# Optimization experiments

Measured on AMD Instinct MI355X. Metric: run time of the kernel, lower is better.

## Reference

```python
import jax, jax.numpy as jnp
import numpy as np

B, N, S, C, H = 16, 64, 4096, 768, 1
HEAD_DIM = C // H
SCALE = HEAD_DIM ** -0.5
ASSIGN_EPS = 1.0


def setup_inputs() -> dict:
    key = jax.random.key(0)
    ks = jax.random.split(key, 8)
    w = lambda k: jax.random.normal(k, (C, C), jnp.float32) * 0.02
    return {
        "query": jax.random.normal(ks[0], (B, N, C), jnp.float32),       # group tokens
        "key_tokens": jax.random.normal(ks[1], (B, S, C), jnp.float32),  # sequence tokens
        "Wq": w(ks[2]), "bq": jnp.zeros((C,), jnp.float32),
        "Wk": w(ks[3]), "bk": jnp.zeros((C,), jnp.float32),
        "Wv": w(ks[4]), "bv": jnp.zeros((C,), jnp.float32),
        "Wo": w(ks[5]), "bo": jnp.zeros((C,), jnp.float32),
    }


def reference(query, key_tokens, Wq, bq, Wk, bk, Wv, bv, Wo, bo):
    # AssignAttention forward (hard=True, gumbel=False -> hard_softmax path).
    def split_heads(x):  # [b, t, C] -> [b, h, t, c]
        b, t, _ = x.shape
        return x.reshape(b, t, H, HEAD_DIM).transpose(0, 2, 1, 3)

    q = split_heads(query @ Wq.T + bq)        # [B, H, N, c]
    k = split_heads(key_tokens @ Wk.T + bk)   # [B, H, S, c]
    v = split_heads(key_tokens @ Wv.T + bv)   # [B, H, S, c]

    raw_attn = jnp.einsum('bhnc,bhsc->bhns', q, k) * SCALE  # [B, H, N, S]

    # hard_softmax over the group (query) dim, axis=-2, with straight-through estimator
    y_soft = jax.nn.softmax(raw_attn, axis=-2)
    idx = jnp.argmax(y_soft, axis=-2)                          # [B, H, S]
    y_hard = jnp.swapaxes(jax.nn.one_hot(idx, N, dtype=raw_attn.dtype), -1, -2)  # [B, H, N, S]
    attn = jax.lax.stop_gradient(y_hard - y_soft) + y_soft

    # sum-renormalization over assigned tokens (sum_assign=False)
    attn = attn / (attn.sum(axis=-1, keepdims=True) + ASSIGN_EPS)

    out = jnp.einsum('bhns,bhsc->bhnc', attn, v)  # [B, H, N, c]
    out = out.transpose(0, 2, 1, 3).reshape(B, N, C)
    return out @ Wo.T + bo
```

## Files before the change

### kernel.cpp

```cpp
#include <hip/hip_runtime.h>
#include <hip/hip_bf16.h>

#define BQ 16
#define NG 64
#define SQ 4096
#define CD 768
#define ROWS (BQ*NG)
#define KSP 4

__global__ __launch_bounds__(256)
void transpose64(const float* __restrict__ src, float* __restrict__ dst,
                 int M, int N)
{
    __shared__ float t[64][65];
    const int bx = blockIdx.x * 64;
    const int by = blockIdx.y * 64;
    const int tx = threadIdx.x & 63, tw = threadIdx.x >> 6;
#pragma unroll
    for (int i = 0; i < 16; ++i) {
        const int row = i * 4 + tw;
        t[row][tx] = src[(size_t)(by + row) * N + bx + tx];
    }
    __syncthreads();
#pragma unroll
    for (int i = 0; i < 16; ++i) {
        const int row = i * 4 + tw;
        dst[(size_t)(bx + row) * M + by + tx] = t[tx][row];
    }
}

__global__ __launch_bounds__(256)
void vecmat3(const float* __restrict__ Wq, const float* __restrict__ bk,
             const float* __restrict__ Wk, const float* __restrict__ bq,
             const float* __restrict__ WoT, const float* __restrict__ bv,
             float* __restrict__ uq, float* __restrict__ bqk,
             float* __restrict__ bvo)
{
    __shared__ float red[4][64];
    const float* Mm; const float* v; float* out;
    if (blockIdx.y == 0)      { Mm = Wq;  v = bk; out = uq;  }
    else if (blockIdx.y == 1) { Mm = Wk;  v = bq; out = bqk; }
    else                      { Mm = WoT; v = bv; out = bvo; }
    const int j0 = blockIdx.x * 64;
    const int jl = threadIdx.x & 63;
    const int cs = threadIdx.x >> 6;
    double a = 0.0;
    for (int c = cs; c < CD; c += 4)
        a += (double)Mm[(size_t)c * CD + j0 + jl] * (double)v[c];
    red[cs][jl] = (float)a;
    __syncthreads();
    if (cs == 0) out[j0 + jl] = red[0][jl] + red[1][jl] + red[2][jl] + red[3][jl];
}

__global__ __launch_bounds__(256)
void delta_q(const float* __restrict__ query, const float* __restrict__ uq,
             const float* __restrict__ bq, const float* __restrict__ bk,
             double* __restrict__ delta)
{
    const int r    = blockIdx.x * 4 + (threadIdx.x >> 6);
    const int lane = threadIdx.x & 63;
    double a = 0.0, b = 0.0;
    for (int c = lane; c < CD; c += 64) {
        a += (double)query[(size_t)r * CD + c] * (double)uq[c];
        b += (double)bq[c] * (double)bk[c];
    }
    a += b;
    for (int off = 32; off; off >>= 1) a += __shfl_down(a, off, 64);
    if (lane == 0) delta[r] = a;
}

__device__ __forceinline__
void gemm_core(const float* __restrict__ AT, int lda,
               const float* __restrict__ B,  int ldb,
               float* __restrict__ Pz, int r0, int c0, int k0, int prow0)
{
    __shared__ float As[64][72];
    __shared__ float Bs[64][72];
    const int tid = threadIdx.x;
    const int c4  = tid & 15;
    const int kr  = tid >> 4;
    const int cg  = tid & 15;
    const int rg  = tid >> 4;

    float  acc[4][4]; double acc64[4][4];
#pragma unroll
    for (int i = 0; i < 4; ++i)
#pragma unroll
        for (int j = 0; j < 4; ++j) { acc[i][j] = 0.f; acc64[i][j] = 0.0; }

    for (int ch = 0; ch < 3; ++ch) {
        const int kb = k0 + ch * 64;
        if (ch) __syncthreads();
#pragma unroll
        for (int i = 0; i < 4; ++i) {
            const int row = i * 16 + kr;
            *(float4*)&As[row][4 * c4] = *(const float4*)(AT + (size_t)(kb + row) * lda + r0 + 4 * c4);
            *(float4*)&Bs[row][4 * c4] = *(const float4*)(B  + (size_t)(kb + row) * ldb + c0 + 4 * c4);
        }
        __syncthreads();
#pragma unroll 8
        for (int dd = 0; dd < 64; ++dd) {
            const float4 a = *(const float4*)&As[dd][4 * rg];
            const float4 b = *(const float4*)&Bs[dd][4 * cg];
            const float av[4] = {a.x, a.y, a.z, a.w};
            const float bv[4] = {b.x, b.y, b.z, b.w};
#pragma unroll
            for (int i = 0; i < 4; ++i)
#pragma unroll
                for (int j = 0; j < 4; ++j) acc[i][j] += av[i] * bv[j];
        }
#pragma unroll
        for (int i = 0; i < 4; ++i)
#pragma unroll
            for (int j = 0; j < 4; ++j) { acc64[i][j] += (double)acc[i][j]; acc[i][j] = 0.f; }
    }
#pragma unroll
    for (int i = 0; i < 4; ++i) {
        const int row = prow0 + 4 * rg + i;
        float4 v;
        v.x = (float)acc64[i][0]; v.y = (float)acc64[i][1];
        v.z = (float)acc64[i][2]; v.w = (float)acc64[i][3];
        *(float4*)(Pz + (size_t)row * CD + c0 + 4 * cg) = v;
    }
}

__global__ __launch_bounds__(256)
void gemm_w(const float* __restrict__ Wq, const float* __restrict__ Wk,
            const float* __restrict__ Wv, const float* __restrict__ WoT,
            float* __restrict__ P)
{
    const int by = blockIdx.y;
    float* Pz = P + (size_t)blockIdx.z * (1536 * CD);
    const float* AT; const float* Bp; int r0;
    if (by < 12) { AT = Wq; Bp = Wk;  r0 = by * 64; }
    else         { AT = Wv; Bp = WoT; r0 = (by - 12) * 64; }
    gemm_core(AT, CD, Bp, CD, Pz, r0, blockIdx.x * 64, blockIdx.z * 192, by * 64);
}

__global__ __launch_bounds__(256)
void gemm_d(const float* __restrict__ AT, const float* __restrict__ B,
            float* __restrict__ P)
{
    float* Pz = P + (size_t)blockIdx.z * (ROWS * CD);
    const int r0 = blockIdx.y * 64;
    gemm_core(AT, ROWS, B, CD, Pz, r0, blockIdx.x * 64, blockIdx.z * 192, r0);
}

__global__ __launch_bounds__(256)
void reduce_sk(const float* __restrict__ P, const float* __restrict__ bias,
               const float* __restrict__ bias2, const int* __restrict__ cnt,
               float* __restrict__ out, int M, int mode)
{
    const int e = blockIdx.x * 256 + threadIdx.x;
    if (e >= M * CD) return;
    const size_t MN = (size_t)M * CD;
    double a = 0.0;
#pragma unroll
    for (int z = 0; z < KSP; ++z) a += (double)P[z * MN + e];
    float v = (float)a;
    if (mode == 1) v += bias[e % CD];
    else if (mode == 3) {
        const int r = e / CD;
        const int cv = cnt[r];
        const float invf = 1.f / ((float)cv + 1.f);
        v = v * invf + ((float)cv * invf) * bias2[e % CD] + bias[e % CD];
    }
    out[e] = v;
}

struct ScoreTiles { float As[64][64]; float Bs[128][64]; };
struct ScoreRed   { double bval[128][17]; int bidx[128][17]; };
union  ScoreShared { ScoreTiles t; ScoreRed r; };

__global__ __launch_bounds__(256)
void score_argmax(const float* __restrict__ gT, const float* __restrict__ key,
                  const double* __restrict__ delta, int* __restrict__ idxo)
{
    __shared__ ScoreShared sh;
    const int tid = threadIdx.x;
    const int b   = blockIdx.y;
    const int s0  = blockIdx.x * 128;
    const int sg  = tid & 15;
    const int ng  = tid >> 4;
    const int c4  = tid & 15;
    const int t4  = tid >> 4;

    float  acc[4][8]; double acc64[4][8];
#pragma unroll
    for (int i = 0; i < 4; ++i)
#pragma unroll
        for (int j = 0; j < 8; ++j) { acc[i][j] = 0.f; acc64[i][j] = 0.0; }

    const float* keyb = key + ((size_t)b * SQ + s0) * CD;
    const float* gTb  = gT + (size_t)b * 64;

    for (int t = 0; t < 12; ++t) {
        const int kb = t * 64;
        __syncthreads();
#pragma unroll
        for (int it = 0; it < 8; ++it) {
            const int row = it * 16 + t4;
            const float4 v = *(const float4*)(keyb + (size_t)row * CD + kb + 4 * c4);
            *(float4*)&sh.t.Bs[row][4 * ((c4 ^ (row >> 3)) & 15)] = v;
        }
#pragma unroll
        for (int it = 0; it < 4; ++it) {
            const int row = it * 16 + t4;
            const float4 v = *(const float4*)(gTb + (size_t)(kb + row) * ROWS + 4 * c4);
            *(float4*)&sh.t.As[row][4 * c4] = v;
        }
        __syncthreads();
#pragma unroll 2
        for (int ddq = 0; ddq < 16; ++ddq) {
            float4 kf[8];
#pragma unroll
            for (int j = 0; j < 8; ++j)
                kf[j] = *(const float4*)&sh.t.Bs[8 * sg + j][4 * ((ddq ^ sg) & 15)];
#pragma unroll
            for (int d = 0; d < 4; ++d) {
                const float4 a = *(const float4*)&sh.t.As[4 * ddq + d][4 * ng];
                const float av[4] = { a.x, a.y, a.z, a.w };
#pragma unroll
                for (int j = 0; j < 8; ++j) {
                    const float kd = (d == 0) ? kf[j].x : (d == 1) ? kf[j].y
                                   : (d == 2) ? kf[j].z : kf[j].w;
#pragma unroll
                    for (int i = 0; i < 4; ++i) acc[i][j] += av[i] * kd;
                }
            }
        }
#pragma unroll
        for (int i = 0; i < 4; ++i)
#pragma unroll
            for (int j = 0; j < 8; ++j) { acc64[i][j] += (double)acc[i][j]; acc[i][j] = 0.f; }
    }

    double dl[4];
#pragma unroll
    for (int i = 0; i < 4; ++i) dl[i] = delta[b * 64 + 4 * ng + i];

    double bv[8]; int bn[8];
#pragma unroll
    for (int j = 0; j < 8; ++j) {
        bv[j] = acc64[0][j] + dl[0]; bn[j] = 4 * ng;
#pragma unroll
        for (int i = 1; i < 4; ++i) {
            const double v = acc64[i][j] + dl[i];
            if (v > bv[j]) { bv[j] = v; bn[j] = 4 * ng + i; }
        }
    }
    __syncthreads();
#pragma unroll
    for (int j = 0; j < 8; ++j) {
        sh.r.bval[8 * sg + j][ng] = bv[j];
        sh.r.bidx[8 * sg + j][ng] = bn[j];
    }
    __syncthreads();
    if (tid < 128) {
        const int s = tid;
        double best = sh.r.bval[s][0]; int bi = sh.r.bidx[s][0];
#pragma unroll
        for (int k = 1; k < 16; ++k) {
            const double v = sh.r.bval[s][k];
            if (v > best) { best = v; bi = sh.r.bidx[s][k]; }
        }
        idxo[b * SQ + s0 + s] = bi;
    }
}

__global__ __launch_bounds__(256)
void gather_ksum(const float* __restrict__ key, const int* __restrict__ idx,
                 float* __restrict__ Ksum, int* __restrict__ cnt)
{
    __shared__ int slist[SQ];
    __shared__ int scount;
    const int n   = blockIdx.x;
    const int b   = blockIdx.y;
    const int tid = threadIdx.x;
    if (tid == 0) scount = 0;
    __syncthreads();

    const int* ib = idx + b * SQ;
#pragma unroll
    for (int p = 0; p < SQ / 256; ++p) {
        const int s = p * 256 + tid;
        if (ib[s] == n) {
            const int pos = atomicAdd(&scount, 1);
            slist[pos] = s;
        }
    }
    __syncthreads();
    const int m = scount;

    double a0 = 0.0, a1 = 0.0, a2 = 0.0;
    const float* kb = key + (size_t)b * SQ * CD;
    const int c1 = tid + 256, c2 = tid + 512;

    int r = 0;
    for (; r + 4 <= m; r += 4) {
        const float* p0 = kb + (size_t)slist[r]     * CD;
        const float* p1 = kb + (size_t)slist[r + 1] * CD;
        const float* p2 = kb + (size_t)slist[r + 2] * CD;
        const float* p3 = kb + (size_t)slist[r + 3] * CD;
        a0 += (double)p0[tid] + (double)p1[tid] + (double)p2[tid] + (double)p3[tid];
        a1 += (double)p0[c1] + (double)p1[c1] + (double)p2[c1] + (double)p3[c1];
        a2 += (double)p0[c2] + (double)p1[c2] + (double)p2[c2] + (double)p3[c2];
    }
    for (; r < m; ++r) {
        const float* p0 = kb + (size_t)slist[r] * CD;
        a0 += (double)p0[tid]; a1 += (double)p0[c1]; a2 += (double)p0[c2];
    }

    float* out = Ksum + (size_t)(b * 64 + n) * CD;
    out[tid] = (float)a0; out[c1] = (float)a1; out[c2] = (float)a2;
    if (tid == 0) cnt[b * 64 + n] = m;
}

extern "C" void kernel_launch(void* const* d_in, const int* in_sizes, int n_in,
                              void* d_out, int out_size, void* d_ws, size_t ws_size,
                              hipStream_t stream)
{
    const float* query = (const float*)d_in[0];
    const float* key   = (const float*)d_in[1];
    const float* Wq    = (const float*)d_in[2];
    const float* bq    = (const float*)d_in[3];
    const float* Wk    = (const float*)d_in[4];
    const float* bk    = (const float*)d_in[5];
    const float* Wv    = (const float*)d_in[6];
    const float* bv    = (const float*)d_in[7];
    const float* Wo    = (const float*)d_in[8];
    const float* bo    = (const float*)d_in[9];

    char* ws = (char*)d_ws;
    const size_t MB = 1 << 20;
    int*    cnt   = (int*)   (ws + 0);
    double* delta = (double*)(ws + 4096);
    float*  uq    = (float*) (ws + 16384);
    float*  bqk   = (float*) (ws + 19456);
    float*  bvo   = (float*) (ws + 22528);
    int*    idx   = (int*)   (ws + 32768);
    float*  qT    = (float*) (ws + 1 * MB);
    float*  WoT   = (float*) (ws + 4 * MB);
    float*  Wqk   = (float*) (ws + 7 * MB);
    float*  Wvo   = Wqk + 768 * 768;
    float*  g     = (float*) (ws + 12 * MB);
    float*  Ksum  = (float*) (ws + 15 * MB);
    float*  KsumT = (float*) (ws + 18 * MB);
    float*  P     = (float*) (ws + 21 * MB);

    transpose64<<<dim3(12, 12), 256, 0, stream>>>(Wo, WoT, CD, CD);
    transpose64<<<dim3(12, 16), 256, 0, stream>>>(query, qT, ROWS, CD);
    vecmat3<<<dim3(12, 3), 256, 0, stream>>>(Wq, bk, Wk, bq, WoT, bv, uq, bqk, bvo);
    delta_q<<<ROWS / 4, 256, 0, stream>>>(query, uq, bq, bk, delta);
    gemm_w<<<dim3(12, 24, KSP), 256, 0, stream>>>(Wq, Wk, Wv, WoT, P);
    reduce_sk<<<(1536 * CD) / 256, 256, 0, stream>>>(P, nullptr, nullptr, nullptr, Wqk, 1536, 0);
    gemm_d<<<dim3(12, 16, KSP), 256, 0, stream>>>(qT, Wqk, P);
    reduce_sk<<<(ROWS * CD) / 256, 256, 0, stream>>>(P, bqk, nullptr, nullptr, g, ROWS, 1);
    float* gT = qT;
    transpose64<<<dim3(12, 16), 256, 0, stream>>>(g, gT, ROWS, CD);
    score_argmax<<<dim3(SQ / 128, BQ), 256, 0, stream>>>(gT, key, delta, idx);
    gather_ksum<<<dim3(NG, BQ), 256, 0, stream>>>(key, idx, Ksum, cnt);
    transpose64<<<dim3(12, 16), 256, 0, stream>>>(Ksum, KsumT, ROWS, CD);
    gemm_d<<<dim3(12, 16, KSP), 256, 0, stream>>>(KsumT, Wvo, P);
    reduce_sk<<<(ROWS * CD) / 256, 256, 0, stream>>>(P, bo, bvo, cnt, (float*)d_out, ROWS, 3);
}
```

Baseline: 643.2 us.

## Rewrite score_argmax with register-resident query slices and per-wave channel split

```diff
diff --git a/kernel.cpp b/kernel.cpp
--- a/kernel.cpp
+++ b/kernel.cpp
@@ -168,103 +168,65 @@
     out[e] = v;
 }
 
-struct ScoreTiles { float As[64][64]; float Bs[128][64]; };
-struct ScoreRed   { double bval[128][17]; int bidx[128][17]; };
-union  ScoreShared { ScoreTiles t; ScoreRed r; };
-
-__global__ __launch_bounds__(256)
+#define STILE 256
+#define SB    16
+
+__global__ __launch_bounds__(768)
 void score_argmax(const float* __restrict__ gT, const float* __restrict__ key,
                   const double* __restrict__ delta, int* __restrict__ idxo)
 {
-    __shared__ ScoreShared sh;
+    __shared__ float  part[SB][12][64];
+    __shared__ double sc[SB][65];
+    __shared__ double dl[64];
+
     const int tid = threadIdx.x;
     const int b   = blockIdx.y;
-    const int s0  = blockIdx.x * 128;
-    const int sg  = tid & 15;
-    const int ng  = tid >> 4;
-    const int c4  = tid & 15;
-    const int t4  = tid >> 4;
-
-    float  acc[4][8]; double acc64[4][8];
-#pragma unroll
-    for (int i = 0; i < 4; ++i)
-#pragma unroll
-        for (int j = 0; j < 8; ++j) { acc[i][j] = 0.f; acc64[i][j] = 0.0; }
-
-    const float* keyb = key + ((size_t)b * SQ + s0) * CD;
-    const float* gTb  = gT + (size_t)b * 64;
-
-    for (int t = 0; t < 12; ++t) {
-        const int kb = t * 64;
+    const int s0  = blockIdx.x * STILE;
+    const int w   = __builtin_amdgcn_readfirstlane(tid >> 6);
+    const int l   = tid & 63;
+
+    if (tid < 64) dl[tid] = delta[b * 64 + tid];
+
+    float greg[64];
+#pragma unroll
+    for (int kk = 0; kk < 64; ++kk)
+        greg[kk] = gT[(size_t)(w * 64 + kk) * ROWS + b * 64 + l];
+
+    const float* keyb = key + (size_t)b * SQ * CD + (size_t)w * 64;
+
+    __syncthreads();
+
+    for (int sb = 0; sb < STILE; sb += SB) {
+        for (int si = 0; si < SB; ++si) {
+            const float* kp = keyb + (size_t)(s0 + sb + si) * CD;
+            float a = 0.f;
+#pragma unroll
+            for (int q = 0; q < 16; ++q) {
+                const float4 kv = *(const float4*)(kp + 4 * q);
+                a += greg[4 * q + 0] * kv.x;
+                a += greg[4 * q + 1] * kv.y;
+                a += greg[4 * q + 2] * kv.z;
+                a += greg[4 * q + 3] * kv.w;
+            }
+            part[si][w][l] = a;
+        }
         __syncthreads();
-#pragma unroll
-        for (int it = 0; it < 8; ++it) {
-            const int row = it * 16 + t4;
-            const float4 v = *(const float4*)(keyb + (size_t)row * CD + kb + 4 * c4);
-            *(float4*)&sh.t.Bs[row][4 * ((c4 ^ (row >> 3)) & 15)] = v;
-        }
-#pragma unroll
-        for (int it = 0; it < 4; ++it) {
-            const int row = it * 16 + t4;
-            const float4 v = *(const float4*)(gTb + (size_t)(kb + row) * ROWS + 4 * c4);
-            *(float4*)&sh.t.As[row][4 * c4] = v;
+        for (int si = w; si < SB; si += 12) {
+            double acc = 0.0;
+#pragma unroll
+            for (int t = 0; t < 12; ++t) acc += (double)part[si][t][l];
+            sc[si][l] = acc + dl[l];
         }
         __syncthreads();
-#pragma unroll 2
-        for (int ddq = 0; ddq < 16; ++ddq) {
-            float4 kf[8];
-#pragma unroll
-            for (int j = 0; j < 8; ++j)
-                kf[j] = *(const float4*)&sh.t.Bs[8 * sg + j][4 * ((ddq ^ sg) & 15)];
-#pragma unroll
-            for (int d = 0; d < 4; ++d) {
-                const float4 a = *(const float4*)&sh.t.As[4 * ddq + d][4 * ng];
-                const float av[4] = { a.x, a.y, a.z, a.w };
-#pragma unroll
-                for (int j = 0; j < 8; ++j) {
-                    const float kd = (d == 0) ? kf[j].x : (d == 1) ? kf[j].y
-                                   : (d == 2) ? kf[j].z : kf[j].w;
-#pragma unroll
-                    for (int i = 0; i < 4; ++i) acc[i][j] += av[i] * kd;
-                }
+        if (tid < SB) {
+            double best = sc[tid][0]; int bi = 0;
+            for (int n = 1; n < 64; ++n) {
+                const double v = sc[tid][n];
+                if (v > best) { best = v; bi = n; }
             }
-        }
-#pragma unroll
-        for (int i = 0; i < 4; ++i)
-#pragma unroll
-            for (int j = 0; j < 8; ++j) { acc64[i][j] += (double)acc[i][j]; acc[i][j] = 0.f; }
-    }
-
-    double dl[4];
-#pragma unroll
-    for (int i = 0; i < 4; ++i) dl[i] = delta[b * 64 + 4 * ng + i];
-
-    double bv[8]; int bn[8];
-#pragma unroll
-    for (int j = 0; j < 8; ++j) {
-        bv[j] = acc64[0][j] + dl[0]; bn[j] = 4 * ng;
-#pragma unroll
-        for (int i = 1; i < 4; ++i) {
-            const double v = acc64[i][j] + dl[i];
-            if (v > bv[j]) { bv[j] = v; bn[j] = 4 * ng + i; }
-        }
-    }
-    __syncthreads();
-#pragma unroll
-    for (int j = 0; j < 8; ++j) {
-        sh.r.bval[8 * sg + j][ng] = bv[j];
-        sh.r.bidx[8 * sg + j][ng] = bn[j];
-    }
-    __syncthreads();
-    if (tid < 128) {
-        const int s = tid;
-        double best = sh.r.bval[s][0]; int bi = sh.r.bidx[s][0];
-#pragma unroll
-        for (int k = 1; k < 16; ++k) {
-            const double v = sh.r.bval[s][k];
-            if (v > best) { best = v; bi = sh.r.bidx[s][k]; }
-        }
-        idxo[b * SQ + s0 + s] = bi;
+            idxo[b * SQ + s0 + sb + tid] = bi;
+        }
+        __syncthreads();
     }
 }
 
@@ -358,7 +320,7 @@
     reduce_sk<<<(ROWS * CD) / 256, 256, 0, stream>>>(P, bqk, nullptr, nullptr, g, ROWS, 1);
     float* gT = qT;
     transpose64<<<dim3(12, 16), 256, 0, stream>>>(g, gT, ROWS, CD);
-    score_argmax<<<dim3(SQ / 128, BQ), 256, 0, stream>>>(gT, key, delta, idx);
+    score_argmax<<<dim3(SQ / STILE, BQ), 768, 0, stream>>>(gT, key, delta, idx);
     gather_ksum<<<dim3(NG, BQ), 256, 0, stream>>>(key, idx, Ksum, cnt);
     transpose64<<<dim3(12, 16), 256, 0, stream>>>(Ksum, KsumT, ROWS, CD);
     gemm_d<<<dim3(12, 16, KSP), 256, 0, stream>>>(KsumT, Wvo, P);
```

Result: slower. 806.6 us (+25.4%).
